# Kernel tuning notes

Measured on AMD Instinct MI355X. Metric: run time of the kernel, lower is better.

## Reference

```python
import math
import jax, jax.numpy as jnp
import numpy as np

N, C, H = 64, 512, 512
SHIFT = 2  # frozen stand-in for random.randint(-3, 3) at module init


def setup_inputs() -> dict:
    key = jax.random.key(0)
    k1, k2, k3 = jax.random.split(key, 3)
    x = jax.random.normal(k1, (N, C, H), dtype=jnp.float32)
    bound = math.sqrt(3.0 / C)
    p1_w = jax.random.uniform(k2, (C, 1), dtype=jnp.float32, minval=-bound, maxval=bound)
    p7_w = 0.02 * jax.random.truncated_normal(k3, -2.0, 2.0, (1, C, H), dtype=jnp.float32)
    return {"x": x, "p1_w": p1_w, "p7_w": p7_w}


def reference(x, p1_w, p7_w):
    n, c, h = x.shape
    inv_sc = 1.0 / math.sqrt(c)
    inv_sh = 1.0 / math.sqrt(h)
    # t1: einsum('abc,bd->adc') with d=1, flattened to (n,h)
    t1 = jnp.einsum('nch,c->nh', x, p1_w[:, 0])
    t2 = jnp.roll(x, SHIFT, axis=1)
    t3 = t1[:, None, :] + t2                     # (n,c,h)
    t4 = x * t3
    t5 = jax.nn.relu(x)
    t7 = p7_w * t5                               # (n,c,h)
    # t8 = softmax(t5^T @ x / sqrt(c))           (n,h,h)
    t8 = jax.nn.softmax(jnp.einsum('nch,ncg->nhg', t5, x) * inv_sc, axis=-1)
    # t9 = t5 @ t4^T / sqrt(h)                   (n,c,c)
    t9 = jnp.einsum('nch,ndh->ncd', t5, t4) * inv_sh
    # t10 = softmax(t7 @ t3^T / sqrt(h))         (n,c,c); (c//g,g) view is cosmetic
    t10 = jax.nn.softmax(jnp.einsum('nch,ndh->ncd', t7, t3) * inv_sh, axis=-1)
    t11 = jnp.minimum(t4, x)
    # t12 = t9^T @ t7 / sqrt(c)                  (n,c,h)
    t12 = jnp.einsum('ndi,ndh->nih', t9, t7) * inv_sc
    # t13 = t11^T @ t2 / sqrt(c)                 (n,h,h)
    t13 = jnp.einsum('nch,ncg->nhg', t11, t2) * inv_sc
    # t14 = softmax(t9^T @ t10^T / sqrt(c))      (n,c,c)
    t14 = jax.nn.softmax(jnp.einsum('nki,njk->nij', t9, t10) * inv_sc, axis=-1)
    # t15 = softmax(t13 @ t8 / sqrt(h))          (n,h,h)
    t15 = jax.nn.softmax(jnp.einsum('nij,njk->nik', t13, t8) * inv_sh, axis=-1)
    # t16 = t12^T @ t14^T / sqrt(c)              (n,h,c)
    t16 = jnp.einsum('nkh,njk->nhj', t12, t14) * inv_sc
    # t17 = t16^T @ t15 / sqrt(h)                (n,c,h)
    t17 = jnp.einsum('nkc,nkj->ncj', t16, t15) * inv_sh
    return t17
```

## Files before the change

### kernel.cpp

```cpp
#include <hip/hip_runtime.h>
#include <math.h>

namespace {

constexpr int kC = 512;
constexpr int kH = 512;
constexpr int kN = 64;
constexpr int kMat = kC * kH;
constexpr float kInvS = 0.04419417382415922f;

enum { SRC_RAW = 0, SRC_X, SRC_T2, SRC_T3, SRC_T4, SRC_T5, SRC_T7, SRC_T11 };

using bf16x8 = __attribute__((ext_vector_type(8))) __bf16;
using f32x4  = __attribute__((ext_vector_type(4))) float;

__device__ __forceinline__ float4 ld4(const float* p) {
  return *reinterpret_cast<const float4*>(p);
}

template <int SRC>
__device__ __forceinline__ float4 elem4(const float* __restrict__ raw,
                                        const float* __restrict__ x,
                                        const float* __restrict__ t1,
                                        const float* __restrict__ p7,
                                        int n, int r, int s) {
  const int nb = n * kMat;
  if constexpr (SRC == SRC_RAW) {
    return ld4(raw + nb + r * kH + s);
  } else if constexpr (SRC == SRC_X) {
    return ld4(x + nb + r * kH + s);
  } else if constexpr (SRC == SRC_T5) {
    float4 v = ld4(x + nb + r * kH + s);
    return make_float4(fmaxf(v.x, 0.f), fmaxf(v.y, 0.f),
                       fmaxf(v.z, 0.f), fmaxf(v.w, 0.f));
  } else if constexpr (SRC == SRC_T7) {
    float4 v = ld4(x + nb + r * kH + s);
    float4 p = ld4(p7 + r * kH + s);
    return make_float4(p.x * fmaxf(v.x, 0.f), p.y * fmaxf(v.y, 0.f),
                       p.z * fmaxf(v.z, 0.f), p.w * fmaxf(v.w, 0.f));
  } else {
    const int rr = (r + kC - 2) & (kC - 1);
    float4 xr = ld4(x + nb + rr * kH + s);
    if constexpr (SRC == SRC_T2) return xr;
    float4 tv = ld4(t1 + n * kH + s);
    float4 t3 = make_float4(tv.x + xr.x, tv.y + xr.y, tv.z + xr.z, tv.w + xr.w);
    if constexpr (SRC == SRC_T3) return t3;
    float4 xv = ld4(x + nb + r * kH + s);
    float4 t4 = make_float4(xv.x * t3.x, xv.y * t3.y, xv.z * t3.z, xv.w * t3.w);
    if constexpr (SRC == SRC_T4) return t4;
    return make_float4(fminf(t4.x, xv.x), fminf(t4.y, xv.y),
                       fminf(t4.z, xv.z), fminf(t4.w, xv.w));
  }
}

template <int SRC>
__device__ __forceinline__ float elem1(const float* __restrict__ raw,
                                       const float* __restrict__ x,
                                       const float* __restrict__ t1,
                                       const float* __restrict__ p7,
                                       int n, int r, int s) {
  const int nb = n * kMat;
  if constexpr (SRC == SRC_RAW) {
    return raw[nb + r * kH + s];
  } else if constexpr (SRC == SRC_X) {
    return x[nb + r * kH + s];
  } else if constexpr (SRC == SRC_T5) {
    return fmaxf(x[nb + r * kH + s], 0.f);
  } else if constexpr (SRC == SRC_T7) {
    return p7[r * kH + s] * fmaxf(x[nb + r * kH + s], 0.f);
  } else {
    const int rr = (r + kC - 2) & (kC - 1);
    float xr = x[nb + rr * kH + s];
    if constexpr (SRC == SRC_T2) return xr;
    float t3 = t1[n * kH + s] + xr;
    if constexpr (SRC == SRC_T3) return t3;
    float xv = x[nb + r * kH + s];
    float t4 = xv * t3;
    if constexpr (SRC == SRC_T4) return t4;
    return fminf(t4, xv);
  }
}

__device__ __forceinline__ unsigned cvtpk(float lo, float hi) {
  unsigned r;
  asm("v_cvt_pk_bf16_f32 %0, %1, %2" : "=v"(r) : "v"(lo), "v"(hi));
  return r;
}

__device__ __forceinline__ void split2(float a, float b, unsigned& q0,
                                       unsigned& q1, unsigned& q2) {
  q0 = cvtpk(a, b);
  float a0 = __builtin_bit_cast(float, q0 << 16);
  float b0 = __builtin_bit_cast(float, q0 & 0xFFFF0000u);
  float ra = a - a0, rb = b - b0;
  q1 = cvtpk(ra, rb);
  float a1 = __builtin_bit_cast(float, q1 << 16);
  float b1 = __builtin_bit_cast(float, q1 & 0xFFFF0000u);
  q2 = cvtpk(ra - a1, rb - b1);
}

constexpr int kPlane = 128 * 32;
constexpr int kMatS = 3 * kPlane;

__device__ __forceinline__ int lds_addr(int r, int ku) {
  int line = r >> 1;
  int slot = ((r & 1) << 2) | (ku >> 3);
  return (line << 6) + ((slot ^ (line & 7)) << 3) + (ku & 7);
}

__device__ __forceinline__ void store3(unsigned short* dst, int r, int ku,
                                       unsigned p0a, unsigned p0b,
                                       unsigned p1a, unsigned p1b,
                                       unsigned p2a, unsigned p2b) {
  int off = lds_addr(r, ku);
  *reinterpret_cast<uint2*>(dst + off)              = make_uint2(p0a, p0b);
  *reinterpret_cast<uint2*>(dst + kPlane + off)     = make_uint2(p1a, p1b);
  *reinterpret_cast<uint2*>(dst + 2 * kPlane + off) = make_uint2(p2a, p2b);
}

template <int SRC, bool TRANS>
__device__ __forceinline__ void stage_tile(unsigned short* dst,
                                           const float* __restrict__ raw,
                                           const float* __restrict__ x,
                                           const float* __restrict__ t1,
                                           const float* __restrict__ p7,
                                           int n, int r0, int k0, int tid) {
  if constexpr (!TRANS) {
#pragma unroll
    for (int i = 0; i < 4; ++i) {
      int e = tid + i * 256;
      int row = e >> 3;
      int k4 = (e & 7) << 2;
      float4 v = elem4<SRC>(raw, x, t1, p7, n, r0 + row, k0 + k4);
      unsigned p0a, p1a, p2a, p0b, p1b, p2b;
      split2(v.x, v.y, p0a, p1a, p2a);
      split2(v.z, v.w, p0b, p1b, p2b);
      store3(dst, row, k4, p0a, p0b, p1a, p1b, p2a, p2b);
    }
  } else {
    const int kb = tid >> 5;
    const int mb = tid & 31;
    float v[4][4];
#pragma unroll
    for (int j = 0; j < 4; ++j)
#pragma unroll
      for (int i = 0; i < 4; ++i)
        v[j][i] = elem1<SRC>(raw, x, t1, p7, n, k0 + kb * 4 + j,
                             r0 + mb + 32 * i);
#pragma unroll
    for (int i = 0; i < 4; ++i) {
      unsigned q0a, q1a, q2a, q0b, q1b, q2b;
      split2(v[0][i], v[1][i], q0a, q1a, q2a);
      split2(v[2][i], v[3][i], q0b, q1b, q2b);
      store3(dst, mb + 32 * i, kb * 4, q0a, q0b, q1a, q1b, q2a, q2b);
    }
  }
}

template <int ASRC, int AT, int BSRC, int BT>
__global__ __launch_bounds__(256, 3) void gemm_kernel(
    const float* __restrict__ Araw, const float* __restrict__ Braw,
    const float* __restrict__ x, const float* __restrict__ t1,
    const float* __restrict__ p7, float* __restrict__ C, float alpha) {
  __shared__ unsigned short smem[2 * kMatS];
  const int n = blockIdx.z;
  const int i0 = blockIdx.y * 128;
  const int j0 = blockIdx.x * 128;
  const int tid = threadIdx.x;
  const int lane = tid & 63;
  const int wid = tid >> 6;
  const int wr = wid >> 1, wc = wid & 1;

  f32x4 acc[4][4];
#pragma unroll
  for (int a = 0; a < 4; ++a)
#pragma unroll
    for (int b = 0; b < 4; ++b) acc[a][b] = (f32x4)0.f;

  const int frow = lane & 15;
  const int kq = (lane >> 4) * 8;

  for (int k0 = 0; k0 < kC; k0 += 32) {
    __syncthreads();
    stage_tile<ASRC, AT == 1>(smem, Araw, x, t1, p7, n, i0, k0, tid);
    stage_tile<BSRC, BT == 0>(smem + kMatS, Braw, x, t1, p7, n, j0, k0, tid);
    __syncthreads();

    bf16x8 B0[4], B1[4], B2[4];
#pragma unroll
    for (int nj = 0; nj < 4; ++nj) {
      int off = kMatS + lds_addr(wc * 64 + nj * 16 + frow, kq);
      B0[nj] = *reinterpret_cast<const bf16x8*>(smem + off);
      B1[nj] = *reinterpret_cast<const bf16x8*>(smem + kPlane + off);
      B2[nj] = *reinterpret_cast<const bf16x8*>(smem + 2 * kPlane + off);
    }
#pragma unroll
    for (int mi = 0; mi < 4; ++mi) {
      int off = lds_addr(wr * 64 + mi * 16 + frow, kq);
      bf16x8 A0 = *reinterpret_cast<const bf16x8*>(smem + off);
      bf16x8 A1 = *reinterpret_cast<const bf16x8*>(smem + kPlane + off);
      bf16x8 A2 = *reinterpret_cast<const bf16x8*>(smem + 2 * kPlane + off);
#pragma unroll
      for (int nj = 0; nj < 4; ++nj) {
        f32x4 c = acc[mi][nj];
        c = __builtin_amdgcn_mfma_f32_16x16x32_bf16(A1, B1[nj], c, 0, 0, 0);
        c = __builtin_amdgcn_mfma_f32_16x16x32_bf16(A0, B2[nj], c, 0, 0, 0);
        c = __builtin_amdgcn_mfma_f32_16x16x32_bf16(A2, B0[nj], c, 0, 0, 0);
        c = __builtin_amdgcn_mfma_f32_16x16x32_bf16(A0, B1[nj], c, 0, 0, 0);
        c = __builtin_amdgcn_mfma_f32_16x16x32_bf16(A1, B0[nj], c, 0, 0, 0);
        c = __builtin_amdgcn_mfma_f32_16x16x32_bf16(A0, B0[nj], c, 0, 0, 0);
        acc[mi][nj] = c;
      }
    }
  }

  const int nb = n * kMat;
  const int rbase = (lane >> 4) * 4;
#pragma unroll
  for (int mi = 0; mi < 4; ++mi) {
#pragma unroll
    for (int nj = 0; nj < 4; ++nj) {
      int row0 = i0 + wr * 64 + mi * 16 + rbase;
      int col = j0 + wc * 64 + nj * 16 + frow;
      float* cp = C + nb + row0 * kH + col;
#pragma unroll
      for (int r = 0; r < 4; ++r) cp[r * kH] = acc[mi][nj][r] * alpha;
    }
  }
}

__global__ __launch_bounds__(256) void t1_kernel(const float* __restrict__ x,
                                                 const float* __restrict__ w,
                                                 float* __restrict__ t1) {
  int idx = blockIdx.x * 256 + threadIdx.x;
  int n = idx >> 9;
  const float* xp = x + n * kMat + (idx & (kH - 1));
  float s = 0.f;
#pragma unroll 8
  for (int c = 0; c < kC; ++c) s = fmaf(xp[c * kH], w[c], s);
  t1[idx] = s;
}

__global__ __launch_bounds__(256) void softmax_kernel(float* __restrict__ buf) {
  __shared__ float red[8];
  float* p = buf + (size_t)blockIdx.x * kH;
  int t = threadIdx.x;
  float2 v = reinterpret_cast<float2*>(p)[t];
  float m = fmaxf(v.x, v.y);
#pragma unroll
  for (int o = 32; o; o >>= 1) m = fmaxf(m, __shfl_xor(m, o));
  if ((t & 63) == 0) red[t >> 6] = m;
  __syncthreads();
  m = fmaxf(fmaxf(red[0], red[1]), fmaxf(red[2], red[3]));
  float e0 = expf(v.x - m), e1 = expf(v.y - m);
  float s = e0 + e1;
#pragma unroll
  for (int o = 32; o; o >>= 1) s += __shfl_xor(s, o);
  __syncthreads();
  if ((t & 63) == 0) red[4 + (t >> 6)] = s;
  __syncthreads();
  s = red[4] + red[5] + red[6] + red[7];
  float inv = 1.f / s;
  reinterpret_cast<float2*>(p)[t] = make_float2(e0 * inv, e1 * inv);
}

}

extern "C" void kernel_launch(void* const* d_in, const int* in_sizes, int n_in,
                              void* d_out, int out_size, void* d_ws,
                              size_t ws_size, hipStream_t stream) {
  (void)in_sizes; (void)n_in; (void)out_size;
  const float* x  = (const float*)d_in[0];
  const float* w  = (const float*)d_in[1];
  const float* p7 = (const float*)d_in[2];
  float* out = (float*)d_out;

  const size_t BUF = (size_t)kN * kMat;
  const size_t need = (4 * BUF + (size_t)kN * kH) * sizeof(float);
  float* ws = (float*)d_ws;
  if (ws_size < need) {
    static float* g_extra = nullptr;
    if (!g_extra) (void)hipMalloc((void**)&g_extra, need);
    ws = g_extra;
  }
  float* b0 = ws;
  float* b1 = b0 + BUF;
  float* b2 = b1 + BUF;
  float* b3 = b2 + BUF;
  float* t1 = b3 + BUF;

  dim3 gg(4, 4, kN);
  dim3 bb(256);
  const int rows = kN * kH;

  t1_kernel<<<rows / 256, bb, 0, stream>>>(x, w, t1);

  gemm_kernel<SRC_T5, 0, SRC_T4, 1><<<gg, bb, 0, stream>>>(nullptr, nullptr, x, t1, p7, b0, kInvS);
  gemm_kernel<SRC_T7, 0, SRC_T3, 1><<<gg, bb, 0, stream>>>(nullptr, nullptr, x, t1, p7, b1, kInvS);
  softmax_kernel<<<rows, bb, 0, stream>>>(b1);
  gemm_kernel<SRC_RAW, 1, SRC_RAW, 1><<<gg, bb, 0, stream>>>(b0, b1, x, t1, p7, b2, kInvS);
  softmax_kernel<<<rows, bb, 0, stream>>>(b2);
  gemm_kernel<SRC_RAW, 1, SRC_T7, 0><<<gg, bb, 0, stream>>>(b0, nullptr, x, t1, p7, b1, kInvS);
  gemm_kernel<SRC_RAW, 1, SRC_RAW, 1><<<gg, bb, 0, stream>>>(b1, b2, x, t1, p7, b0, kInvS);
  gemm_kernel<SRC_T11, 1, SRC_T2, 0><<<gg, bb, 0, stream>>>(nullptr, nullptr, x, t1, p7, b1, kInvS);
  gemm_kernel<SRC_T5, 1, SRC_X, 0><<<gg, bb, 0, stream>>>(nullptr, nullptr, x, t1, p7, b2, kInvS);
  softmax_kernel<<<rows, bb, 0, stream>>>(b2);
  gemm_kernel<SRC_RAW, 0, SRC_RAW, 0><<<gg, bb, 0, stream>>>(b1, b2, x, t1, p7, b3, kInvS);
  softmax_kernel<<<rows, bb, 0, stream>>>(b3);
  gemm_kernel<SRC_RAW, 1, SRC_RAW, 0><<<gg, bb, 0, stream>>>(b0, b3, x, t1, p7, out, kInvS);
}
```

Before: 1.355 ms.

## Prefetch next K tile into registers and vectorize transposed staging loads

Splits tile staging into a global-load phase and an LDS-write phase, so the global loads for the next K slice are issued before the MFMA work on the current slice and their latency overlaps with compute. The transposed staging path now reads float4 vectors along the contiguous dimension instead of scalar strided elements, and each thread owns four adjacent rows. This costs 32 extra live float registers per thread under launch_bounds(256,3), which may cause spilling or lower occupancy.

```diff
diff --git a/kernel.cpp b/kernel.cpp
--- a/kernel.cpp
+++ b/kernel.cpp
@@ -53,34 +53,6 @@
   }
 }
 
-template <int SRC>
-__device__ __forceinline__ float elem1(const float* __restrict__ raw,
-                                       const float* __restrict__ x,
-                                       const float* __restrict__ t1,
-                                       const float* __restrict__ p7,
-                                       int n, int r, int s) {
-  const int nb = n * kMat;
-  if constexpr (SRC == SRC_RAW) {
-    return raw[nb + r * kH + s];
-  } else if constexpr (SRC == SRC_X) {
-    return x[nb + r * kH + s];
-  } else if constexpr (SRC == SRC_T5) {
-    return fmaxf(x[nb + r * kH + s], 0.f);
-  } else if constexpr (SRC == SRC_T7) {
-    return p7[r * kH + s] * fmaxf(x[nb + r * kH + s], 0.f);
-  } else {
-    const int rr = (r + kC - 2) & (kC - 1);
-    float xr = x[nb + rr * kH + s];
-    if constexpr (SRC == SRC_T2) return xr;
-    float t3 = t1[n * kH + s] + xr;
-    if constexpr (SRC == SRC_T3) return t3;
-    float xv = x[nb + r * kH + s];
-    float t4 = xv * t3;
-    if constexpr (SRC == SRC_T4) return t4;
-    return fminf(t4, xv);
-  }
-}
-
 __device__ __forceinline__ unsigned cvtpk(float lo, float hi) {
   unsigned r;
   asm("v_cvt_pk_bf16_f32 %0, %1, %2" : "=v"(r) : "v"(lo), "v"(hi));
@@ -119,7 +91,7 @@
 }
 
 template <int SRC, bool TRANS>
-__device__ __forceinline__ void stage_tile(unsigned short* dst,
+__device__ __forceinline__ void stage_load(float v[4][4],
                                            const float* __restrict__ raw,
                                            const float* __restrict__ x,
                                            const float* __restrict__ t1,
@@ -127,32 +99,42 @@
                                            int n, int r0, int k0, int tid) {
   if constexpr (!TRANS) {
 #pragma unroll
-    for (int i = 0; i < 4; ++i) {
-      int e = tid + i * 256;
-      int row = e >> 3;
-      int k4 = (e & 7) << 2;
-      float4 v = elem4<SRC>(raw, x, t1, p7, n, r0 + row, k0 + k4);
+    for (int u = 0; u < 4; ++u) {
+      int e = tid + u * 256;
+      float4 t = elem4<SRC>(raw, x, t1, p7, n, r0 + (e >> 3),
+                            k0 + ((e & 7) << 2));
+      v[u][0] = t.x; v[u][1] = t.y; v[u][2] = t.z; v[u][3] = t.w;
+    }
+  } else {
+    int kb = tid >> 5, mb = tid & 31;
+#pragma unroll
+    for (int j = 0; j < 4; ++j) {
+      float4 t = elem4<SRC>(raw, x, t1, p7, n, k0 + kb * 4 + j, r0 + mb * 4);
+      v[j][0] = t.x; v[j][1] = t.y; v[j][2] = t.z; v[j][3] = t.w;
+    }
+  }
+}
+
+template <bool TRANS>
+__device__ __forceinline__ void stage_write(unsigned short* dst,
+                                            const float v[4][4], int tid) {
+  if constexpr (!TRANS) {
+#pragma unroll
+    for (int u = 0; u < 4; ++u) {
+      int e = tid + u * 256;
       unsigned p0a, p1a, p2a, p0b, p1b, p2b;
-      split2(v.x, v.y, p0a, p1a, p2a);
-      split2(v.z, v.w, p0b, p1b, p2b);
-      store3(dst, row, k4, p0a, p0b, p1a, p1b, p2a, p2b);
+      split2(v[u][0], v[u][1], p0a, p1a, p2a);
+      split2(v[u][2], v[u][3], p0b, p1b, p2b);
+      store3(dst, e >> 3, (e & 7) << 2, p0a, p0b, p1a, p1b, p2a, p2b);
     }
   } else {
-    const int kb = tid >> 5;
-    const int mb = tid & 31;
-    float v[4][4];
-#pragma unroll
-    for (int j = 0; j < 4; ++j)
-#pragma unroll
-      for (int i = 0; i < 4; ++i)
-        v[j][i] = elem1<SRC>(raw, x, t1, p7, n, k0 + kb * 4 + j,
-                             r0 + mb + 32 * i);
+    int kb = tid >> 5, mb = tid & 31;
 #pragma unroll
     for (int i = 0; i < 4; ++i) {
       unsigned q0a, q1a, q2a, q0b, q1b, q2b;
       split2(v[0][i], v[1][i], q0a, q1a, q2a);
       split2(v[2][i], v[3][i], q0b, q1b, q2b);
-      store3(dst, mb + 32 * i, kb * 4, q0a, q0b, q1a, q1b, q2a, q2b);
+      store3(dst, mb * 4 + i, kb * 4, q0a, q0b, q1a, q1b, q2a, q2b);
     }
   }
 }
@@ -180,11 +162,18 @@
   const int frow = lane & 15;
   const int kq = (lane >> 4) * 8;
 
+  float vA[4][4], vB[4][4];
+  stage_load<ASRC, AT == 1>(vA, Araw, x, t1, p7, n, i0, 0, tid);
+  stage_load<BSRC, BT == 0>(vB, Braw, x, t1, p7, n, j0, 0, tid);
+
   for (int k0 = 0; k0 < kC; k0 += 32) {
+    stage_write<AT == 1>(smem, vA, tid);
+    stage_write<BT == 0>(smem + kMatS, vB, tid);
     __syncthreads();
-    stage_tile<ASRC, AT == 1>(smem, Araw, x, t1, p7, n, i0, k0, tid);
-    stage_tile<BSRC, BT == 0>(smem + kMatS, Braw, x, t1, p7, n, j0, k0, tid);
-    __syncthreads();
+    if (k0 + 32 < kC) {
+      stage_load<ASRC, AT == 1>(vA, Araw, x, t1, p7, n, i0, k0 + 32, tid);
+      stage_load<BSRC, BT == 0>(vB, Braw, x, t1, p7, n, j0, k0 + 32, tid);
+    }
 
     bf16x8 B0[4], B1[4], B2[4];
 #pragma unroll
@@ -212,6 +201,7 @@
         acc[mi][nj] = c;
       }
     }
+    __syncthreads();
   }
 
   const int nb = n * kMat;
```

Measured after the change: 2.738 ms. 2.02x slower.
